# Kernel optimization log

Measured on AMD Instinct MI355X. Metric: run time of the kernel, lower is better.

## Reference

```python
import jax, jax.numpy as jnp
import numpy as np

N, C_TOTAL, C, H, W = 8, 448, 100, 56, 56


def setup_inputs() -> dict:
    key = jax.random.key(0)
    k1, k2, k3, k4 = jax.random.split(key, 4)
    fmaps = jax.random.normal(k1, (N, C_TOTAL, H, W), dtype=jnp.float32)
    select_index = jax.random.randint(k2, (C,), 0, C_TOTAL)
    mean = jax.random.normal(k3, (C, H, W), dtype=jnp.float32)
    # Per-pixel inverse covariance must be PSD so the quadratic form is >= 0
    A = jax.random.normal(k4, (C, C, H, W), dtype=jnp.float32)
    cov = jnp.einsum('cehw,dehw->cdhw', A, A) / jnp.float32(C)  # (C,C,H,W), PSD per pixel
    return {
        'fmaps': fmaps,
        'select_index': select_index,
        'mean': mean,
        'cov': cov,
        'min_score': jnp.float32(0.0),
        'max_score': jnp.float32(50.0),
    }


def reference(fmaps, select_index, mean, cov, min_score, max_score):
    # x_ = fmaps[:, select_index, ...] - mean  -> (N, C, H, W)
    x = fmaps[:, select_index, :, :] - mean[None]
    # left = sum_c x[n,c,h,w] * cov[c,d,h,w]  (per-pixel matvec), avoids (N,C,C,H,W) intermediate
    left = jnp.einsum('nchw,cdhw->ndhw', x, cov)
    # per-pixel Mahalanobis distance
    s_map = jnp.sqrt(jnp.sum(x * left, axis=1))  # (N, H, W)
    # bilinear upsample x4 (torch Upsample align_corners=False == half-pixel linear resize)
    score_map = jax.image.resize(s_map, (s_map.shape[0], 4 * H, 4 * W), method='linear')
    scores = (score_map - min_score) / (max_score - min_score)
    return jnp.squeeze(scores)
```

## Files before the change

### kernel.cpp

```cpp
#include <hip/hip_runtime.h>
#include <math.h>

#define NN 8
#define C_TOTAL 448
#define CC 100
#define HH 56
#define WW 56
#define HW (HH*WW)
#define NPIX4 (HW/4)
#define OH 224
#define OW 224
#define NT4 13
#define NK 50

typedef __attribute__((ext_vector_type(4))) _Float16 half4;
typedef __attribute__((ext_vector_type(8))) _Float16 half8;

__device__ __forceinline__ void fma4(float4& acc, const float4 a, const float4 b) {
    acc.x = fmaf(a.x, b.x, acc.x);
    acc.y = fmaf(a.y, b.y, acc.y);
    acc.z = fmaf(a.z, b.z, acc.z);
    acc.w = fmaf(a.w, b.w, acc.w);
}
__device__ __forceinline__ float4 h2f(const half4 h) {
    float4 r; r.x = (float)h.x; r.y = (float)h.y; r.z = (float)h.z; r.w = (float)h.w;
    return r;
}

__global__ __launch_bounds__(256) void prep_x_kernel(
    const float* __restrict__ fmaps, const int* __restrict__ sel,
    const float* __restrict__ mean, half4* __restrict__ xbuf,
    float* __restrict__ smap)
{
    const int idx = blockIdx.x * 256 + threadIdx.x;
    if (idx < NN * NPIX4) {
        ((float4*)smap)[idx] = make_float4(0.f, 0.f, 0.f, 0.f);
    }
    if (idx >= CC * NPIX4) return;
    const int quad = idx % NPIX4;
    const int c    = idx / NPIX4;

    const float4* f4 = (const float4*)fmaps;
    const float4  m  = ((const float4*)mean)[(size_t)c * NPIX4 + quad];
    const int     sc = sel[c];

    half4 hv[NN];
#pragma unroll
    for (int n = 0; n < NN; ++n) {
        const float4 f = f4[((size_t)n * C_TOTAL + sc) * NPIX4 + quad];
        half4 h;
        h.x = (_Float16)(f.x - m.x);
        h.y = (_Float16)(f.y - m.y);
        h.z = (_Float16)(f.z - m.z);
        h.w = (_Float16)(f.w - m.w);
        hv[n] = h;
    }
    half4* dst = xbuf + ((size_t)c * NPIX4 + quad) * NN;
#pragma unroll
    for (int n = 0; n < NN; ++n) dst[n] = hv[n];
}

__global__ __launch_bounds__(512, 4) void qform_kernel(
    const half4* __restrict__ xbuf, const float* __restrict__ cov,
    float* __restrict__ smap)
{
    __shared__ float4 lred[NN * NN * 64];

    const int tile = blockIdx.x % NT4;
    const int k    = blockIdx.x / NT4;
    const int a    = 2 * k;
    const int b    = a + 1;
    const int w    = threadIdx.x >> 6;
    const int lane = threadIdx.x & 63;
    const int qraw = tile * 64 + lane;
    const bool valid = qraw < NPIX4;
    const int quad = valid ? qraw : (NPIX4 - 1);

    const float4* c4 = (const float4*)cov;

    float4 acca[NN], accb[NN];
#pragma unroll
    for (int n = 0; n < NN; ++n) {
        acca[n] = make_float4(0.f, 0.f, 0.f, 0.f);
        accb[n] = make_float4(0.f, 0.f, 0.f, 0.f);
    }

    for (int d = a + w; d < CC; d += NN) {
        const half8* xp = (const half8*)(xbuf + ((size_t)d * NPIX4 + quad) * NN);
        const half8 p0 = xp[0];
        const half8 p1 = xp[1];
        const half8 p2 = xp[2];
        const half8 p3 = xp[3];
        float4 xv[NN];
        xv[0] = make_float4((float)p0[0], (float)p0[1], (float)p0[2], (float)p0[3]);
        xv[1] = make_float4((float)p0[4], (float)p0[5], (float)p0[6], (float)p0[7]);
        xv[2] = make_float4((float)p1[0], (float)p1[1], (float)p1[2], (float)p1[3]);
        xv[3] = make_float4((float)p1[4], (float)p1[5], (float)p1[6], (float)p1[7]);
        xv[4] = make_float4((float)p2[0], (float)p2[1], (float)p2[2], (float)p2[3]);
        xv[5] = make_float4((float)p2[4], (float)p2[5], (float)p2[6], (float)p2[7]);
        xv[6] = make_float4((float)p3[0], (float)p3[1], (float)p3[2], (float)p3[3]);
        xv[7] = make_float4((float)p3[4], (float)p3[5], (float)p3[6], (float)p3[7]);

        float4 cva = c4[((size_t)a * CC + d) * NPIX4 + quad];
        if (d == a) { cva.x *= 0.5f; cva.y *= 0.5f; cva.z *= 0.5f; cva.w *= 0.5f; }
#pragma unroll
        for (int n = 0; n < NN; ++n) fma4(acca[n], xv[n], cva);

        if (d > a) {
            float4 cvb = c4[((size_t)b * CC + d) * NPIX4 + quad];
            if (d == b) { cvb.x *= 0.5f; cvb.y *= 0.5f; cvb.z *= 0.5f; cvb.w *= 0.5f; }
#pragma unroll
            for (int n = 0; n < NN; ++n) fma4(accb[n], xv[n], cvb);
        }
    }

    const half4* xap = xbuf + ((size_t)a * NPIX4 + quad) * NN;
    const half4* xbp = xbuf + ((size_t)b * NPIX4 + quad) * NN;
#pragma unroll
    for (int n = 0; n < NN; ++n) {
        const float4 xa = h2f(xap[n]);
        const float4 xb = h2f(xbp[n]);
        float4 t;
        t.x = 2.f * fmaf(xb.x, accb[n].x, xa.x * acca[n].x);
        t.y = 2.f * fmaf(xb.y, accb[n].y, xa.y * acca[n].y);
        t.z = 2.f * fmaf(xb.z, accb[n].z, xa.z * acca[n].z);
        t.w = 2.f * fmaf(xb.w, accb[n].w, xa.w * acca[n].w);
        lred[(w * NN + n) * 64 + lane] = t;
    }
    __syncthreads();

    {
        const int n = w;
        float4 sum = make_float4(0.f, 0.f, 0.f, 0.f);
#pragma unroll
        for (int ww = 0; ww < NN; ++ww) {
            const float4 v = lred[(ww * NN + n) * 64 + lane];
            sum.x += v.x; sum.y += v.y; sum.z += v.z; sum.w += v.w;
        }
        if (valid) {
            float* dst = smap + (size_t)n * HW + (size_t)qraw * 4;
            atomicAdd(dst + 0, sum.x);
            atomicAdd(dst + 1, sum.y);
            atomicAdd(dst + 2, sum.z);
            atomicAdd(dst + 3, sum.w);
        }
    }
}

__global__ __launch_bounds__(256) void upsample_kernel(
    const float* __restrict__ smap,
    const float* __restrict__ minp, const float* __restrict__ maxp,
    float* __restrict__ out)
{
    const int idx = blockIdx.x * 256 + threadIdx.x;
    const int total = NN * OH * OW;
    if (idx >= total) return;

    const int ox = idx % OW;
    const int oy = (idx / OW) % OH;
    const int n  = idx / (OW * OH);

    const float fy = oy * 0.25f - 0.375f;
    const float fx = ox * 0.25f - 0.375f;

    int y0 = (int)floorf(fy);
    int x0 = (int)floorf(fx);
    const float wy = fy - (float)y0;
    const float wx = fx - (float)x0;
    int y1 = min(y0 + 1, HH - 1); y0 = max(y0, 0);
    int x1 = min(x0 + 1, WW - 1); x0 = max(x0, 0);

    const float* s = smap + (size_t)n * HW;
    const float v00 = sqrtf(fmaxf(s[y0 * WW + x0], 0.f));
    const float v01 = sqrtf(fmaxf(s[y0 * WW + x1], 0.f));
    const float v10 = sqrtf(fmaxf(s[y1 * WW + x0], 0.f));
    const float v11 = sqrtf(fmaxf(s[y1 * WW + x1], 0.f));

    const float v = (1.0f - wy) * ((1.0f - wx) * v00 + wx * v01)
                  +          wy * ((1.0f - wx) * v10 + wx * v11);

    const float mn = *minp;
    const float mx = *maxp;
    out[idx] = (v - mn) / (mx - mn);
}

extern "C" void kernel_launch(void* const* d_in, const int* in_sizes, int n_in,
                              void* d_out, int out_size, void* d_ws, size_t ws_size,
                              hipStream_t stream)
{
    const float* fmaps = (const float*)d_in[0];
    const int*   sel   = (const int*)  d_in[1];
    const float* mean  = (const float*)d_in[2];
    const float* cov   = (const float*)d_in[3];
    const float* minp  = (const float*)d_in[4];
    const float* maxp  = (const float*)d_in[5];
    float* out = (float*)d_out;

    half4* xbuf = (half4*)d_ws;
    float* smap = (float*)((char*)d_ws + (size_t)CC*NPIX4*NN*8);

    {
        const int total = CC * NPIX4;
        prep_x_kernel<<<(total + 255) / 256, 256, 0, stream>>>(fmaps, sel, mean, xbuf, smap);
    }
    qform_kernel<<<NT4 * NK, 512, 0, stream>>>(xbuf, cov, smap);
    {
        const int total = NN * OH * OW;
        upsample_kernel<<<(total + 255) / 256, 256, 0, stream>>>(smap, minp, maxp, out);
    }
}
```

Baseline: 216.3 us.

## Split qform work across batch halves and d-range halves with smaller blocks

The quadratic-form kernel now uses 256-thread blocks. Each block's d-range is split into two halves across separate blocks, and within a block the waves are split over d parity and batch halves, so each thread keeps only 4 batch accumulators instead of 8. This doubles the grid and lowers register pressure to raise occupancy. Cov loads use nontemporal hints because cov is streamed once. In exchange, the xbuf loads are duplicated across waves and more atomic adds go to smap.

```diff
diff --git a/kernel.cpp b/kernel.cpp
--- a/kernel.cpp
+++ b/kernel.cpp
@@ -15,15 +15,20 @@
 
 typedef __attribute__((ext_vector_type(4))) _Float16 half4;
 typedef __attribute__((ext_vector_type(8))) _Float16 half8;
-
-__device__ __forceinline__ void fma4(float4& acc, const float4 a, const float4 b) {
-    acc.x = fmaf(a.x, b.x, acc.x);
-    acc.y = fmaf(a.y, b.y, acc.y);
-    acc.z = fmaf(a.z, b.z, acc.z);
-    acc.w = fmaf(a.w, b.w, acc.w);
-}
-__device__ __forceinline__ float4 h2f(const half4 h) {
-    float4 r; r.x = (float)h.x; r.y = (float)h.y; r.z = (float)h.z; r.w = (float)h.w;
+typedef __attribute__((ext_vector_type(4))) float    f32x4;
+
+__device__ __forceinline__ f32x4 cvtlo(const half8 h) {
+    return __builtin_convertvector(__builtin_shufflevector(h, h, 0, 1, 2, 3), f32x4);
+}
+__device__ __forceinline__ f32x4 cvthi(const half8 h) {
+    return __builtin_convertvector(__builtin_shufflevector(h, h, 4, 5, 6, 7), f32x4);
+}
+__device__ __forceinline__ f32x4 fmav(const f32x4 a, const f32x4 b, const f32x4 c) {
+    f32x4 r;
+    r.x = fmaf(a.x, b.x, c.x);
+    r.y = fmaf(a.y, b.y, c.y);
+    r.z = fmaf(a.z, b.z, c.z);
+    r.w = fmaf(a.w, b.w, c.w);
     return r;
 }
 
@@ -60,89 +65,94 @@
     for (int n = 0; n < NN; ++n) dst[n] = hv[n];
 }
 
-__global__ __launch_bounds__(512, 4) void qform_kernel(
+__global__ __launch_bounds__(256, 5) void qform_kernel(
     const half4* __restrict__ xbuf, const float* __restrict__ cov,
     float* __restrict__ smap)
 {
-    __shared__ float4 lred[NN * NN * 64];
+    __shared__ f32x4 lred[4 * 4 * 64];
 
     const int tile = blockIdx.x % NT4;
-    const int k    = blockIdx.x / NT4;
+    const int rest = blockIdx.x / NT4;
+    const int h    = rest & 1;
+    const int k    = rest >> 1;
     const int a    = 2 * k;
     const int b    = a + 1;
+
     const int w    = threadIdx.x >> 6;
+    const int dph  = w & 1;
+    const int nh   = w >> 1;
     const int lane = threadIdx.x & 63;
     const int qraw = tile * 64 + lane;
     const bool valid = qraw < NPIX4;
     const int quad = valid ? qraw : (NPIX4 - 1);
 
-    const float4* c4 = (const float4*)cov;
-
-    float4 acca[NN], accb[NN];
-#pragma unroll
-    for (int n = 0; n < NN; ++n) {
-        acca[n] = make_float4(0.f, 0.f, 0.f, 0.f);
-        accb[n] = make_float4(0.f, 0.f, 0.f, 0.f);
-    }
-
-    for (int d = a + w; d < CC; d += NN) {
-        const half8* xp = (const half8*)(xbuf + ((size_t)d * NPIX4 + quad) * NN);
-        const half8 p0 = xp[0];
-        const half8 p1 = xp[1];
-        const half8 p2 = xp[2];
-        const half8 p3 = xp[3];
-        float4 xv[NN];
-        xv[0] = make_float4((float)p0[0], (float)p0[1], (float)p0[2], (float)p0[3]);
-        xv[1] = make_float4((float)p0[4], (float)p0[5], (float)p0[6], (float)p0[7]);
-        xv[2] = make_float4((float)p1[0], (float)p1[1], (float)p1[2], (float)p1[3]);
-        xv[3] = make_float4((float)p1[4], (float)p1[5], (float)p1[6], (float)p1[7]);
-        xv[4] = make_float4((float)p2[0], (float)p2[1], (float)p2[2], (float)p2[3]);
-        xv[5] = make_float4((float)p2[4], (float)p2[5], (float)p2[6], (float)p2[7]);
-        xv[6] = make_float4((float)p3[0], (float)p3[1], (float)p3[2], (float)p3[3]);
-        xv[7] = make_float4((float)p3[4], (float)p3[5], (float)p3[6], (float)p3[7]);
-
-        float4 cva = c4[((size_t)a * CC + d) * NPIX4 + quad];
-        if (d == a) { cva.x *= 0.5f; cva.y *= 0.5f; cva.z *= 0.5f; cva.w *= 0.5f; }
-#pragma unroll
-        for (int n = 0; n < NN; ++n) fma4(acca[n], xv[n], cva);
+    const int L   = CC - a;
+    const int mid = a + ((L + 1) >> 1);
+    const int dlo = h ? mid : a;
+    const int dhi = h ? CC  : mid;
+
+    const f32x4* c4 = (const f32x4*)cov;
+
+    f32x4 acca[4], accb[4];
+#pragma unroll
+    for (int i = 0; i < 4; ++i) {
+        acca[i] = (f32x4){0.f, 0.f, 0.f, 0.f};
+        accb[i] = (f32x4){0.f, 0.f, 0.f, 0.f};
+    }
+
+    for (int d = dlo + dph; d < dhi; d += 2) {
+        const half8* xp = (const half8*)(xbuf + ((size_t)d * NPIX4 + quad) * NN + nh * 4);
+        const half8 hA = xp[0];
+        const half8 hB = xp[1];
+        f32x4 xv[4];
+        xv[0] = cvtlo(hA); xv[1] = cvthi(hA);
+        xv[2] = cvtlo(hB); xv[3] = cvthi(hB);
+
+        f32x4 cva = __builtin_nontemporal_load(&c4[((size_t)a * CC + d) * NPIX4 + quad]);
+        if (d == a) cva *= 0.5f;
+#pragma unroll
+        for (int i = 0; i < 4; ++i) acca[i] = fmav(xv[i], cva, acca[i]);
 
         if (d > a) {
-            float4 cvb = c4[((size_t)b * CC + d) * NPIX4 + quad];
-            if (d == b) { cvb.x *= 0.5f; cvb.y *= 0.5f; cvb.z *= 0.5f; cvb.w *= 0.5f; }
-#pragma unroll
-            for (int n = 0; n < NN; ++n) fma4(accb[n], xv[n], cvb);
+            f32x4 cvb = __builtin_nontemporal_load(&c4[((size_t)b * CC + d) * NPIX4 + quad]);
+            if (d == b) cvb *= 0.5f;
+#pragma unroll
+            for (int i = 0; i < 4; ++i) accb[i] = fmav(xv[i], cvb, accb[i]);
         }
     }
 
-    const half4* xap = xbuf + ((size_t)a * NPIX4 + quad) * NN;
-    const half4* xbp = xbuf + ((size_t)b * NPIX4 + quad) * NN;
-#pragma unroll
-    for (int n = 0; n < NN; ++n) {
-        const float4 xa = h2f(xap[n]);
-        const float4 xb = h2f(xbp[n]);
-        float4 t;
-        t.x = 2.f * fmaf(xb.x, accb[n].x, xa.x * acca[n].x);
-        t.y = 2.f * fmaf(xb.y, accb[n].y, xa.y * acca[n].y);
-        t.z = 2.f * fmaf(xb.z, accb[n].z, xa.z * acca[n].z);
-        t.w = 2.f * fmaf(xb.w, accb[n].w, xa.w * acca[n].w);
-        lred[(w * NN + n) * 64 + lane] = t;
+    {
+        const half8* xap = (const half8*)(xbuf + ((size_t)a * NPIX4 + quad) * NN + nh * 4);
+        const half8* xbp = (const half8*)(xbuf + ((size_t)b * NPIX4 + quad) * NN + nh * 4);
+        const half8 xa0 = xap[0], xa1 = xap[1];
+        const half8 xb0 = xbp[0], xb1 = xbp[1];
+        f32x4 xa[4], xb[4];
+        xa[0] = cvtlo(xa0); xa[1] = cvthi(xa0); xa[2] = cvtlo(xa1); xa[3] = cvthi(xa1);
+        xb[0] = cvtlo(xb0); xb[1] = cvthi(xb0); xb[2] = cvtlo(xb1); xb[3] = cvthi(xb1);
+#pragma unroll
+        for (int i = 0; i < 4; ++i) {
+            f32x4 t = xa[i] * acca[i];
+            t = fmav(xb[i], accb[i], t);
+            t = t + t;
+            lred[(w * 4 + i) * 64 + lane] = t;
+        }
     }
     __syncthreads();
 
-    {
-        const int n = w;
-        float4 sum = make_float4(0.f, 0.f, 0.f, 0.f);
-#pragma unroll
-        for (int ww = 0; ww < NN; ++ww) {
-            const float4 v = lred[(ww * NN + n) * 64 + lane];
-            sum.x += v.x; sum.y += v.y; sum.z += v.z; sum.w += v.w;
-        }
+#pragma unroll
+    for (int j = 0; j < 2; ++j) {
+        const int im  = 2 * w + j;
+        const int nhh = im >> 2;
+        const int sl  = im & 3;
+        const f32x4 s0 = lred[((nhh * 2 + 0) * 4 + sl) * 64 + lane];
+        const f32x4 s1 = lred[((nhh * 2 + 1) * 4 + sl) * 64 + lane];
+        const f32x4 s  = s0 + s1;
         if (valid) {
-            float* dst = smap + (size_t)n * HW + (size_t)qraw * 4;
-            atomicAdd(dst + 0, sum.x);
-            atomicAdd(dst + 1, sum.y);
-            atomicAdd(dst + 2, sum.z);
-            atomicAdd(dst + 3, sum.w);
+            float* dst = smap + (size_t)im * HW + (size_t)qraw * 4;
+            atomicAdd(dst + 0, s.x);
+            atomicAdd(dst + 1, s.y);
+            atomicAdd(dst + 2, s.z);
+            atomicAdd(dst + 3, s.w);
         }
     }
 }
@@ -203,7 +213,7 @@
         const int total = CC * NPIX4;
         prep_x_kernel<<<(total + 255) / 256, 256, 0, stream>>>(fmaps, sel, mean, xbuf, smap);
     }
-    qform_kernel<<<NT4 * NK, 512, 0, stream>>>(xbuf, cov, smap);
+    qform_kernel<<<NK * 2 * NT4, 256, 0, stream>>>(xbuf, cov, smap);
     {
         const int total = NN * OH * OW;
         upsample_kernel<<<(total + 255) / 256, 256, 0, stream>>>(smap, minp, maxp, out);
```

After: 233.5 us. 1.08x slower.
